# Optimization experiments

Measured on AMD Instinct MI355X. Metric: run time of the kernel, lower is better.

The kernel has to match this reference:

```python
import jax, jax.numpy as jnp
import numpy as np

N_NODES = 50000
N_EDGES = 800000
IN_DIM = 5
HID = (32, 64, 128, 64, 32)
OUT_DIM = 2
EPS = 1e-5  # nn.BatchNorm1d default eps


def _bn(x, g, b):
    # BatchNorm1d in training mode: batch (biased) statistics over nodes
    m = jnp.mean(x, axis=0)
    v = jnp.var(x, axis=0)
    return (x - m) * jax.lax.rsqrt(v + EPS) * g + b


def setup_inputs() -> dict:
    key = jax.random.key(0)
    ks = jax.random.split(key, 40)
    it = iter(range(40))
    def nrm(shape, s=0.1):
        return jax.random.normal(ks[next(it)], shape, jnp.float32) * s
    inp = {}
    inp["x"] = jax.random.normal(ks[next(it)], (N_NODES, IN_DIM), jnp.float32)
    inp["edge_index"] = jax.random.randint(ks[next(it)], (2, N_EDGES), 0, N_NODES, jnp.int32)
    # input embedding: Linear(5,32) -> ReLU -> BatchNorm1d(32)
    inp["emb_W"] = nrm((IN_DIM, HID[0]))
    inp["emb_b"] = jnp.zeros((HID[0],), jnp.float32)
    inp["emb_g"] = jnp.ones((HID[0],), jnp.float32)
    inp["emb_beta"] = jnp.zeros((HID[0],), jnp.float32)
    # 4 GraphConv blocks
    for i in range(len(HID) - 1):
        din, dout = HID[i], HID[i + 1]
        inp[f"b{i}_Wrel"] = nrm((din, dout))   # lin_rel weight (has bias)
        inp[f"b{i}_brel"] = jnp.zeros((dout,), jnp.float32)
        inp[f"b{i}_Wroot"] = nrm((din, dout))  # lin_root weight (no bias)
        inp[f"b{i}_g"] = jnp.ones((dout,), jnp.float32)
        inp[f"b{i}_beta"] = jnp.zeros((dout,), jnp.float32)
    # output MLP: Linear(32,16) -> ReLU -> Linear(16,2)
    inp["out_W1"] = nrm((HID[-1], HID[-1] // 2))
    inp["out_b1"] = jnp.zeros((HID[-1] // 2,), jnp.float32)
    inp["out_W2"] = nrm((HID[-1] // 2, OUT_DIM))
    inp["out_b2"] = jnp.zeros((OUT_DIM,), jnp.float32)
    return inp


def reference(x, edge_index,
              emb_W, emb_b, emb_g, emb_beta,
              b0_Wrel, b0_brel, b0_Wroot, b0_g, b0_beta,
              b1_Wrel, b1_brel, b1_Wroot, b1_g, b1_beta,
              b2_Wrel, b2_brel, b2_Wroot, b2_g, b2_beta,
              b3_Wrel, b3_brel, b3_Wroot, b3_g, b3_beta,
              out_W1, out_b1, out_W2, out_b2):
    src, dst = edge_index[0], edge_index[1]
    # input embedding: Linear -> ReLU -> BN
    h = jnp.maximum(x @ emb_W + emb_b, 0.0)
    h = _bn(h, emb_g, emb_beta)
    blocks = [
        (b0_Wrel, b0_brel, b0_Wroot, b0_g, b0_beta),
        (b1_Wrel, b1_brel, b1_Wroot, b1_g, b1_beta),
        (b2_Wrel, b2_brel, b2_Wroot, b2_g, b2_beta),
        (b3_Wrel, b3_brel, b3_Wroot, b3_g, b3_beta),
    ]
    for Wrel, brel, Wroot, g, beta in blocks:
        # GraphConv (aggr='add'): lin_rel(sum_{j in N(i)} x_j) + lin_root(x_i)
        agg = jax.ops.segment_sum(h[src], dst, num_segments=N_NODES)
        h = agg @ Wrel + brel + h @ Wroot
        # BN then ReLU (GNNBlock order)
        h = jnp.maximum(_bn(h, g, beta), 0.0)
    # output MLP
    h = jnp.maximum(h @ out_W1 + out_b1, 0.0)
    return h @ out_W2 + out_b2
```

## Files before the change

### kernel.cpp

```cpp
#include <hip/hip_runtime.h>

#define N_NODES 50000
#define N_EDGES 800000
#define BN_EPS 1e-5f

__device__ __forceinline__ void fma4(float4& a, float s, const float4& w) {
    a.x += s * w.x; a.y += s * w.y; a.z += s * w.z; a.w += s * w.w;
}
__device__ __forceinline__ void add4(float4& a, const float4& b) {
    a.x += b.x; a.y += b.y; a.z += b.z; a.w += b.w;
}

template <int NY>
__device__ __forceinline__ bool xcd_decode(int nx, int& x, int& y) {
    const int s = blockIdx.x & (8 * NY - 1);
    const int g = blockIdx.x / (8 * NY);
    x = g * 8 + (s & 7);
    y = s >> 3;
    return x < nx;
}
static inline int xcd_grid(int nx, int ny) { return ((nx + 7) / 8 * 8) * ny; }

__global__ void zero_i(int* __restrict__ p, int n) {
    int i = blockIdx.x * blockDim.x + threadIdx.x;
    int stride = gridDim.x * blockDim.x;
    for (; i < n; i += stride) p[i] = 0;
}

__global__ void hist_kernel(const int* __restrict__ dst, int* __restrict__ cnt) {
    int i = blockIdx.x * blockDim.x + threadIdx.x;
    int stride = gridDim.x * blockDim.x;
    for (; i < N_EDGES; i += stride) atomicAdd(&cnt[dst[i]], 1);
}
__global__ void scan1_kernel(const int* __restrict__ cnt, int* __restrict__ rp,
                             int* __restrict__ bsum) {
    __shared__ int s[256];
    int t = threadIdx.x;
    int idx = blockIdx.x * 256 + t;
    int v = (idx < N_NODES) ? cnt[idx] : 0;
    s[t] = v;
    __syncthreads();
    for (int off = 1; off < 256; off <<= 1) {
        int x = 0;
        if (t >= off) x = s[t - off];
        __syncthreads();
        s[t] += x;
        __syncthreads();
    }
    if (idx < N_NODES) rp[idx] = s[t] - v;
    if (t == 255) bsum[blockIdx.x] = s[255];
}
__global__ void scan2_kernel(int* __restrict__ bsum, int nb, float* __restrict__ stats) {
    __shared__ int s[256];
    int t = threadIdx.x;
    for (int i = t; i < 5 * 256; i += 256) stats[i] = 0.f;
    int v = (t < nb) ? bsum[t] : 0;
    s[t] = v;
    __syncthreads();
    for (int off = 1; off < 256; off <<= 1) {
        int x = 0;
        if (t >= off) x = s[t - off];
        __syncthreads();
        s[t] += x;
        __syncthreads();
    }
    if (t < nb) bsum[t] = s[t] - v;
}
__global__ void scan3_kernel(int* __restrict__ rp, const int* __restrict__ bsum,
                             int* __restrict__ cnt) {
    int idx = blockIdx.x * 256 + threadIdx.x;
    if (idx < N_NODES) {
        rp[idx] += bsum[blockIdx.x];
        cnt[idx] = 0;
    }
    if (idx == 0) rp[N_NODES] = N_EDGES;
}
__global__ void fill_kernel(const int* __restrict__ src, const int* __restrict__ dst,
                            const int* __restrict__ rp, int* __restrict__ cur,
                            int* __restrict__ ssrc) {
    int i = blockIdx.x * blockDim.x + threadIdx.x;
    int stride = gridDim.x * blockDim.x;
    for (; i < N_EDGES; i += stride) {
        int d = dst[i];
        int p = rp[d] + atomicAdd(&cur[d], 1);
        ssrc[p] = src[i];
    }
}

__global__ __launch_bounds__(256) void emb_fused(
    const float* __restrict__ x, const float* __restrict__ W,
    const float* __restrict__ b, float* __restrict__ out,
    float* __restrict__ stats) {
    __shared__ float lsum[32], lssq[32];
    if (threadIdx.x < 32) { lsum[threadIdx.x] = 0.f; lssq[threadIdx.x] = 0.f; }
    __syncthreads();
    const int o = threadIdx.x & 31;
    const int total = N_NODES * 32;
    float mys = 0.f, myq = 0.f;
    for (int base = blockIdx.x * 256; base < total; base += gridDim.x * 256) {
        int idx = base + threadIdx.x;
        float acc = 0.f;
        if (idx < total) {
            int n = idx >> 5;
            const float* xr = x + n * 5;
            acc = b[o];
#pragma unroll
            for (int k = 0; k < 5; ++k) acc += xr[k] * W[k * 32 + o];
            acc = fmaxf(acc, 0.f);
            out[idx] = acc;
        }
        mys += acc;
        myq += acc * acc;
    }
    mys += __shfl_xor(mys, 32);
    myq += __shfl_xor(myq, 32);
    if ((threadIdx.x & 63) < 32) { atomicAdd(&lsum[o], mys); atomicAdd(&lssq[o], myq); }
    __syncthreads();
    if (threadIdx.x < 32) {
        atomicAdd(&stats[threadIdx.x], lsum[threadIdx.x]);
        atomicAdd(&stats[32 + threadIdx.x], lssq[threadIdx.x]);
    }
}

template <int D>
__device__ __forceinline__ void bn_finalize_lds(
    const float* __restrict__ stats, const float* __restrict__ g,
    const float* __restrict__ beta, float* sc, float* sh) {
    const float invN = 1.f / (float)N_NODES;
    for (int f = threadIdx.x; f < D; f += 256) {
        float m = stats[f] * invN;
        float var = stats[D + f] * invN - m * m;
        float a = g[f] * rsqrtf(var + BN_EPS);
        sc[f] = a;
        sh[f] = beta[f] - m * a;
    }
    __syncthreads();
}

__global__ __launch_bounds__(256) void bn_apply(
    float4* __restrict__ h, const float* __restrict__ g,
    const float* __restrict__ beta, const float* __restrict__ stats,
    int logD, int relu) {
    const int D = 1 << logD;
    const int total4 = N_NODES << (logD - 2);
    const float invN = 1.f / (float)N_NODES;
    int idx = blockIdx.x * blockDim.x + threadIdx.x;
    int stride = gridDim.x * blockDim.x;
    for (; idx < total4; idx += stride) {
        int f = (idx & ((D >> 2) - 1)) << 2;
        float4 v = h[idx];
        float* vp = (float*)&v;
#pragma unroll
        for (int c = 0; c < 4; ++c) {
            float m = stats[f + c] * invN;
            float var = stats[D + f + c] * invN - m * m;
            float y = (vp[c] - m) * rsqrtf(var + BN_EPS) * g[f + c] + beta[f + c];
            if (relu) y = fmaxf(y, 0.f);
            vp[c] = y;
        }
        h[idx] = v;
    }
}

template <int LOGD>
__global__ __launch_bounds__(256) void gather_agg(
    const float* __restrict__ h, const int* __restrict__ rp,
    const int* __restrict__ ssrc, float4* __restrict__ agg) {
    constexpr int QSH = LOGD - 2;
    int tid = blockIdx.x * 256 + threadIdx.x;
    int node = tid >> QSH;
    if (node >= N_NODES) return;
    int q = tid & ((1 << QSH) - 1);
    int e0 = rp[node], e1 = rp[node + 1];
    float4 acc = make_float4(0.f, 0.f, 0.f, 0.f);
    int e = e0;
    for (; e + 4 <= e1; e += 4) {
        int s0 = ssrc[e], s1 = ssrc[e + 1], s2 = ssrc[e + 2], s3 = ssrc[e + 3];
        float4 v0 = ((const float4*)(h + ((size_t)s0 << LOGD)))[q];
        float4 v1 = ((const float4*)(h + ((size_t)s1 << LOGD)))[q];
        float4 v2 = ((const float4*)(h + ((size_t)s2 << LOGD)))[q];
        float4 v3 = ((const float4*)(h + ((size_t)s3 << LOGD)))[q];
        add4(v0, v1); add4(v2, v3); add4(acc, v0); add4(acc, v2);
    }
    for (; e < e1; ++e) {
        float4 v = ((const float4*)(h + ((size_t)ssrc[e] << LOGD)))[q];
        add4(acc, v);
    }
    agg[tid] = acc;
}

template <int DIN, int DOUT, int OBL>
__global__ __launch_bounds__(256) void gconv_bn0(
    const float* __restrict__ h, const float* __restrict__ agg,
    const float* __restrict__ Wrel, const float* __restrict__ brel,
    const float* __restrict__ Wroot, float* __restrict__ out,
    const float* __restrict__ stats_in, const float* __restrict__ g_in,
    const float* __restrict__ beta_in, const int* __restrict__ deg,
    float* __restrict__ stats_out, int nx) {
    constexpr int NY = 2;
    constexpr int LPN = OBL / 4;
    constexpr int SLOTS = 256 / LPN;
    constexpr int NPT = 4;
    constexpr int KS = 8;
    constexpr int TOT4 = DIN * OBL / 4;
    int bx, by;
    if (!xcd_decode<NY>(nx, bx, by)) return;
    __shared__ __align__(16) float wl[2 * DIN * OBL];
    __shared__ __align__(16) float sc[DIN];
    __shared__ __align__(16) float sh[DIN];
    __shared__ float lsum[OBL], lssq[OBL];
    const int ob0 = by * OBL;
    for (int e4 = threadIdx.x; e4 < TOT4; e4 += 256) {
        int k = e4 / (OBL / 4);
        int j = (e4 % (OBL / 4)) * 4;
        ((float4*)wl)[e4] = *(const float4*)(Wrel + (size_t)k * DOUT + ob0 + j);
        ((float4*)wl)[TOT4 + e4] = *(const float4*)(Wroot + (size_t)k * DOUT + ob0 + j);
    }
    if (threadIdx.x < OBL) { lsum[threadIdx.x] = 0.f; lssq[threadIdx.x] = 0.f; }
    bn_finalize_lds<DIN>(stats_in, g_in, beta_in, sc, sh);

    const int q = threadIdx.x & (LPN - 1);
    const int slot = threadIdx.x / LPN;
    const int o0 = ob0 + q * 4;
    const int nbase = bx * (SLOTS * NPT) + slot;

    float degf[NPT];
#pragma unroll
    for (int i = 0; i < NPT; ++i) {
        int n = nbase + i * SLOTS;
        degf[i] = (n < N_NODES) ? (float)deg[n] : 0.f;
    }

    float4 bias = *(const float4*)(brel + o0);
    float4 acc[NPT];
#pragma unroll
    for (int i = 0; i < NPT; ++i) acc[i] = bias;

#pragma unroll 1
    for (int s = 0; s < DIN / KS; ++s) {
        const int k0 = s * KS;
        float4 s2[2] = {((const float4*)sc)[k0 / 4], ((const float4*)sc)[k0 / 4 + 1]};
        float4 t2[2] = {((const float4*)sh)[k0 / 4], ((const float4*)sh)[k0 / 4 + 1]};
        const float* scp = (const float*)s2;
        const float* shp = (const float*)t2;
        float4 hv[NPT][2], av[NPT][2];
#pragma unroll
        for (int i = 0; i < NPT; ++i) {
            int n = nbase + i * SLOTS;
            int nn = (n < N_NODES) ? n : 0;
            const float4* hr = (const float4*)(h + (size_t)nn * DIN + k0);
            const float4* ar = (const float4*)(agg + (size_t)nn * DIN + k0);
            hv[i][0] = hr[0]; hv[i][1] = hr[1];
            av[i][0] = ar[0]; av[i][1] = ar[1];
        }
#pragma unroll
        for (int kk = 0; kk < KS; ++kk) {
            float4 wr = *(const float4*)&wl[(k0 + kk) * OBL + q * 4];
            float4 wo = *(const float4*)&wl[DIN * OBL + (k0 + kk) * OBL + q * 4];
#pragma unroll
            for (int i = 0; i < NPT; ++i) {
                float a  = fmaf(((const float*)av[i])[kk], scp[kk], degf[i] * shp[kk]);
                float hh = fmaf(((const float*)hv[i])[kk], scp[kk], shp[kk]);
                fma4(acc[i], a, wr);
                fma4(acc[i], hh, wo);
            }
        }
    }
#pragma unroll
    for (int i = 0; i < NPT; ++i) {
        int n = nbase + i * SLOTS;
        if (n < N_NODES)
            *(float4*)(out + (size_t)n * DOUT + o0) = acc[i];
        else
            acc[i] = make_float4(0.f, 0.f, 0.f, 0.f);
    }
    float4 s4 = make_float4(0.f, 0.f, 0.f, 0.f);
    float4 q4 = make_float4(0.f, 0.f, 0.f, 0.f);
#pragma unroll
    for (int i = 0; i < NPT; ++i) {
        s4.x += acc[i].x; s4.y += acc[i].y; s4.z += acc[i].z; s4.w += acc[i].w;
        q4.x += acc[i].x * acc[i].x; q4.y += acc[i].y * acc[i].y;
        q4.z += acc[i].z * acc[i].z; q4.w += acc[i].w * acc[i].w;
    }
#pragma unroll
    for (int d = LPN; d < 64; d <<= 1) {
        s4.x += __shfl_xor(s4.x, d); s4.y += __shfl_xor(s4.y, d);
        s4.z += __shfl_xor(s4.z, d); s4.w += __shfl_xor(s4.w, d);
        q4.x += __shfl_xor(q4.x, d); q4.y += __shfl_xor(q4.y, d);
        q4.z += __shfl_xor(q4.z, d); q4.w += __shfl_xor(q4.w, d);
    }
    if ((threadIdx.x & 63) < LPN) {
        int c = q * 4;
        atomicAdd(&lsum[c + 0], s4.x); atomicAdd(&lsum[c + 1], s4.y);
        atomicAdd(&lsum[c + 2], s4.z); atomicAdd(&lsum[c + 3], s4.w);
        atomicAdd(&lssq[c + 0], q4.x); atomicAdd(&lssq[c + 1], q4.y);
        atomicAdd(&lssq[c + 2], q4.z); atomicAdd(&lssq[c + 3], q4.w);
    }
    __syncthreads();
    if (threadIdx.x < OBL) {
        atomicAdd(&stats_out[ob0 + threadIdx.x], lsum[threadIdx.x]);
        atomicAdd(&stats_out[DOUT + ob0 + threadIdx.x], lssq[threadIdx.x]);
    }
}

template <int DIN, int DOUT, int OBL>
__global__ __launch_bounds__(256) void gconv_lds(
    const float* __restrict__ h, const float* __restrict__ agg,
    const float* __restrict__ Wrel, const float* __restrict__ brel,
    const float* __restrict__ Wroot, float* __restrict__ out,
    float* __restrict__ stats_out, int nx) {
    constexpr int NY = DOUT / OBL;
    constexpr int LPN = OBL / 4;
    constexpr int SLOTS = 256 / LPN;
    constexpr int NPT = 4;
    constexpr int KS = 8;
    constexpr int TOT4 = DIN * OBL / 4;
    int bx, by;
    if (!xcd_decode<NY>(nx, bx, by)) return;
    __shared__ __align__(16) float wl[2 * DIN * OBL];
    __shared__ float lsum[OBL], lssq[OBL];
    const int ob0 = by * OBL;
    for (int e4 = threadIdx.x; e4 < TOT4; e4 += 256) {
        int k = e4 / (OBL / 4);
        int j = (e4 % (OBL / 4)) * 4;
        ((float4*)wl)[e4] = *(const float4*)(Wrel + (size_t)k * DOUT + ob0 + j);
        ((float4*)wl)[TOT4 + e4] = *(const float4*)(Wroot + (size_t)k * DOUT + ob0 + j);
    }
    if (threadIdx.x < OBL) { lsum[threadIdx.x] = 0.f; lssq[threadIdx.x] = 0.f; }
    __syncthreads();

    const int q = threadIdx.x & (LPN - 1);
    const int slot = threadIdx.x / LPN;
    const int o0 = ob0 + q * 4;
    const int nbase = bx * (SLOTS * NPT) + slot;

    float4 bias = *(const float4*)(brel + o0);
    float4 acc[NPT];
#pragma unroll
    for (int i = 0; i < NPT; ++i) acc[i] = bias;

#pragma unroll 1
    for (int s = 0; s < DIN / KS; ++s) {
        const int k0 = s * KS;
        float4 hv[NPT][2], av[NPT][2];
#pragma unroll
        for (int i = 0; i < NPT; ++i) {
            int n = nbase + i * SLOTS;
            int nn = (n < N_NODES) ? n : 0;
            const float4* hr = (const float4*)(h + (size_t)nn * DIN + k0);
            const float4* ar = (const float4*)(agg + (size_t)nn * DIN + k0);
            hv[i][0] = hr[0]; hv[i][1] = hr[1];
            av[i][0] = ar[0]; av[i][1] = ar[1];
        }
#pragma unroll
        for (int kk = 0; kk < KS; ++kk) {
            float4 wr = *(const float4*)&wl[(k0 + kk) * OBL + q * 4];
            float4 wo = *(const float4*)&wl[DIN * OBL + (k0 + kk) * OBL + q * 4];
#pragma unroll
            for (int i = 0; i < NPT; ++i) {
                fma4(acc[i], ((const float*)av[i])[kk], wr);
                fma4(acc[i], ((const float*)hv[i])[kk], wo);
            }
        }
    }
#pragma unroll
    for (int i = 0; i < NPT; ++i) {
        int n = nbase + i * SLOTS;
        if (n < N_NODES)
            *(float4*)(out + (size_t)n * DOUT + o0) = acc[i];
        else
            acc[i] = make_float4(0.f, 0.f, 0.f, 0.f);
    }
    float4 s4 = make_float4(0.f, 0.f, 0.f, 0.f);
    float4 q4 = make_float4(0.f, 0.f, 0.f, 0.f);
#pragma unroll
    for (int i = 0; i < NPT; ++i) {
        s4.x += acc[i].x; s4.y += acc[i].y; s4.z += acc[i].z; s4.w += acc[i].w;
        q4.x += acc[i].x * acc[i].x; q4.y += acc[i].y * acc[i].y;
        q4.z += acc[i].z * acc[i].z; q4.w += acc[i].w * acc[i].w;
    }
#pragma unroll
    for (int d = LPN; d < 64; d <<= 1) {
        s4.x += __shfl_xor(s4.x, d); s4.y += __shfl_xor(s4.y, d);
        s4.z += __shfl_xor(s4.z, d); s4.w += __shfl_xor(s4.w, d);
        q4.x += __shfl_xor(q4.x, d); q4.y += __shfl_xor(q4.y, d);
        q4.z += __shfl_xor(q4.z, d); q4.w += __shfl_xor(q4.w, d);
    }
    if ((threadIdx.x & 63) < LPN) {
        int c = q * 4;
        atomicAdd(&lsum[c + 0], s4.x); atomicAdd(&lsum[c + 1], s4.y);
        atomicAdd(&lsum[c + 2], s4.z); atomicAdd(&lsum[c + 3], s4.w);
        atomicAdd(&lssq[c + 0], q4.x); atomicAdd(&lssq[c + 1], q4.y);
        atomicAdd(&lssq[c + 2], q4.z); atomicAdd(&lssq[c + 3], q4.w);
    }
    __syncthreads();
    if (threadIdx.x < OBL) {
        atomicAdd(&stats_out[ob0 + threadIdx.x], lsum[threadIdx.x]);
        atomicAdd(&stats_out[DOUT + ob0 + threadIdx.x], lssq[threadIdx.x]);
    }
}

template <int DIN, int DOUT, int OBL>
__global__ __launch_bounds__(256) void prem_bn(
    const float* __restrict__ h, const float* __restrict__ Wrel,
    const float* __restrict__ brel, const float* __restrict__ Wroot,
    float* __restrict__ P, float* __restrict__ Q,
    const float* __restrict__ stats_in, const float* __restrict__ g_in,
    const float* __restrict__ beta_in, int nx) {
    constexpr int NY = DOUT / OBL;
    constexpr int LPN = OBL / 4;
    constexpr int SLOTS = 256 / LPN;
    constexpr int NPT = 4;
    constexpr int KS = 8;
    constexpr int TOT4 = DIN * OBL / 4;
    int bx, by;
    if (!xcd_decode<NY>(nx, bx, by)) return;
    __shared__ __align__(16) float wl[2 * DIN * OBL];
    __shared__ __align__(16) float sc[DIN];
    __shared__ __align__(16) float sh[DIN];
    const int ob0 = by * OBL;
    for (int e4 = threadIdx.x; e4 < TOT4; e4 += 256) {
        int k = e4 / (OBL / 4);
        int j = (e4 % (OBL / 4)) * 4;
        ((float4*)wl)[e4] = *(const float4*)(Wrel + (size_t)k * DOUT + ob0 + j);
        ((float4*)wl)[TOT4 + e4] = *(const float4*)(Wroot + (size_t)k * DOUT + ob0 + j);
    }
    bn_finalize_lds<DIN>(stats_in, g_in, beta_in, sc, sh);

    const int q = threadIdx.x & (LPN - 1);
    const int slot = threadIdx.x / LPN;
    const int o0 = ob0 + q * 4;
    const int nbase = bx * (SLOTS * NPT) + slot;

    float4 bias = *(const float4*)(brel + o0);
    float4 accp[NPT], accq[NPT];
#pragma unroll
    for (int i = 0; i < NPT; ++i) {
        accp[i] = make_float4(0.f, 0.f, 0.f, 0.f);
        accq[i] = bias;
    }

#pragma unroll 1
    for (int s = 0; s < DIN / KS; ++s) {
        const int k0 = s * KS;
        float4 s2[2] = {((const float4*)sc)[k0 / 4], ((const float4*)sc)[k0 / 4 + 1]};
        float4 t2[2] = {((const float4*)sh)[k0 / 4], ((const float4*)sh)[k0 / 4 + 1]};
        const float* scp = (const float*)s2;
        const float* shp = (const float*)t2;
        float4 hv[NPT][2];
#pragma unroll
        for (int i = 0; i < NPT; ++i) {
            int n = nbase + i * SLOTS;
            int nn = (n < N_NODES) ? n : 0;
            const float4* hr = (const float4*)(h + (size_t)nn * DIN + k0);
            hv[i][0] = hr[0]; hv[i][1] = hr[1];
        }
#pragma unroll
        for (int kk = 0; kk < KS; ++kk) {
            float4 wr = *(const float4*)&wl[(k0 + kk) * OBL + q * 4];
            float4 wo = *(const float4*)&wl[DIN * OBL + (k0 + kk) * OBL + q * 4];
#pragma unroll
            for (int i = 0; i < NPT; ++i) {
                float hh = fmaxf(fmaf(((const float*)hv[i])[kk], scp[kk], shp[kk]), 0.f);
                fma4(accp[i], hh, wr);
                fma4(accq[i], hh, wo);
            }
        }
    }
#pragma unroll
    for (int i = 0; i < NPT; ++i) {
        int n = nbase + i * SLOTS;
        if (n < N_NODES) {
            *(float4*)(P + (size_t)n * DOUT + o0) = accp[i];
            *(float4*)(Q + (size_t)n * DOUT + o0) = accq[i];
        }
    }
}

template <int LOGD>
__global__ __launch_bounds__(256) void gather_add_fused(
    const float* __restrict__ P, const int* __restrict__ rp,
    const int* __restrict__ ssrc, float4* __restrict__ out,
    float* __restrict__ stats) {
    constexpr int D = 1 << LOGD;
    constexpr int Q4 = D / 4;
    __shared__ float lsum[D], lssq[D];
    if (threadIdx.x < D) { lsum[threadIdx.x] = 0.f; lssq[threadIdx.x] = 0.f; }
    __syncthreads();

    const int total = N_NODES * Q4;
    const int q = threadIdx.x & (Q4 - 1);
    float4 mys = make_float4(0.f, 0.f, 0.f, 0.f);
    float4 myq = make_float4(0.f, 0.f, 0.f, 0.f);

    for (int base = blockIdx.x * 256; base < total; base += gridDim.x * 256) {
        int tid = base + threadIdx.x;
        float4 acc = make_float4(0.f, 0.f, 0.f, 0.f);
        if (tid < total) {
            int node = tid >> (LOGD - 2);
            int e0 = rp[node], e1 = rp[node + 1];
            acc = out[tid];
            int e = e0;
            for (; e + 4 <= e1; e += 4) {
                int s0 = ssrc[e], s1 = ssrc[e + 1], s2 = ssrc[e + 2], s3 = ssrc[e + 3];
                float4 v0 = ((const float4*)(P + ((size_t)s0 << LOGD)))[q];
                float4 v1 = ((const float4*)(P + ((size_t)s1 << LOGD)))[q];
                float4 v2 = ((const float4*)(P + ((size_t)s2 << LOGD)))[q];
                float4 v3 = ((const float4*)(P + ((size_t)s3 << LOGD)))[q];
                add4(v0, v1); add4(v2, v3); add4(acc, v0); add4(acc, v2);
            }
            for (; e < e1; ++e) {
                float4 v = ((const float4*)(P + ((size_t)ssrc[e] << LOGD)))[q];
                add4(acc, v);
            }
            out[tid] = acc;
        }
        mys.x += acc.x; mys.y += acc.y; mys.z += acc.z; mys.w += acc.w;
        myq.x += acc.x * acc.x; myq.y += acc.y * acc.y;
        myq.z += acc.z * acc.z; myq.w += acc.w * acc.w;
    }
#pragma unroll
    for (int d = Q4; d < 64; d <<= 1) {
        mys.x += __shfl_xor(mys.x, d); mys.y += __shfl_xor(mys.y, d);
        mys.z += __shfl_xor(mys.z, d); mys.w += __shfl_xor(mys.w, d);
        myq.x += __shfl_xor(myq.x, d); myq.y += __shfl_xor(myq.y, d);
        myq.z += __shfl_xor(myq.z, d); myq.w += __shfl_xor(myq.w, d);
    }
    if ((threadIdx.x & 63) < Q4) {
        atomicAdd(&lsum[4 * q + 0], mys.x); atomicAdd(&lsum[4 * q + 1], mys.y);
        atomicAdd(&lsum[4 * q + 2], mys.z); atomicAdd(&lsum[4 * q + 3], mys.w);
        atomicAdd(&lssq[4 * q + 0], myq.x); atomicAdd(&lssq[4 * q + 1], myq.y);
        atomicAdd(&lssq[4 * q + 2], myq.z); atomicAdd(&lssq[4 * q + 3], myq.w);
    }
    __syncthreads();
    if (threadIdx.x < D) {
        atomicAdd(&stats[threadIdx.x], lsum[threadIdx.x]);
        atomicAdd(&stats[D + threadIdx.x], lssq[threadIdx.x]);
    }
}

__global__ __launch_bounds__(256) void outmlp_kernel(
    const float* __restrict__ h, const float* __restrict__ stats,
    const float* __restrict__ g, const float* __restrict__ beta,
    const float* __restrict__ W1, const float* __restrict__ b1,
    const float* __restrict__ W2, const float* __restrict__ b2,
    float* __restrict__ out) {
    int n = blockIdx.x * 256 + threadIdx.x;
    if (n >= N_NODES) return;
    const float invN = 1.f / (float)N_NODES;
    const float4* hr4 = (const float4*)(h + (size_t)n * 32);
    float hv[32];
#pragma unroll
    for (int k4 = 0; k4 < 8; ++k4) {
        float4 v = hr4[k4];
        float* vp = (float*)&v;
#pragma unroll
        for (int c = 0; c < 4; ++c) {
            int f = 4 * k4 + c;
            float m = stats[f] * invN;
            float var = stats[32 + f] * invN - m * m;
            hv[f] = fmaxf((vp[c] - m) * rsqrtf(var + BN_EPS) * g[f] + beta[f], 0.f);
        }
    }
    float hid[16];
#pragma unroll
    for (int j = 0; j < 16; ++j) hid[j] = b1[j];
#pragma unroll
    for (int k = 0; k < 32; ++k) {
        float hk = hv[k];
#pragma unroll
        for (int j = 0; j < 16; ++j) hid[j] += hk * W1[k * 16 + j];
    }
    float o0 = b2[0], o1 = b2[1];
#pragma unroll
    for (int j = 0; j < 16; ++j) {
        float t = fmaxf(hid[j], 0.f);
        o0 += t * W2[j * 2 + 0];
        o1 += t * W2[j * 2 + 1];
    }
    out[n * 2 + 0] = o0;
    out[n * 2 + 1] = o1;
}

extern "C" void kernel_launch(void* const* d_in, const int* in_sizes, int n_in,
                              void* d_out, int out_size, void* d_ws, size_t ws_size,
                              hipStream_t stream) {
    const float* x        = (const float*)d_in[0];
    const int*   ei       = (const int*)d_in[1];
    const int*   src      = ei;
    const int*   dst      = ei + N_EDGES;
    const float* emb_W    = (const float*)d_in[2];
    const float* emb_b    = (const float*)d_in[3];
    const float* emb_g    = (const float*)d_in[4];
    const float* emb_beta = (const float*)d_in[5];
    const float* out_W1   = (const float*)d_in[26];
    const float* out_b1   = (const float*)d_in[27];
    const float* out_W2   = (const float*)d_in[28];
    const float* out_b2   = (const float*)d_in[29];

    float* ws = (float*)d_ws;
    const size_t HMAX = (size_t)N_NODES * 128;
    float* hA    = ws;
    float* hB    = ws + HMAX;
    float* P     = ws + 2 * HMAX;
    float* stats = ws + 2 * HMAX + (size_t)N_NODES * 64;
    int*   rp    = (int*)(stats + 5 * 256);
    int*   cnt   = rp + N_NODES + 1;
    int*   bsum  = cnt + N_NODES;
    int*   ssrc  = bsum + 256;

    float* st0 = stats;
    float* st1 = stats + 256;
    float* st2 = stats + 512;
    float* st3 = stats + 768;
    float* st4 = stats + 1024;

    const int BS = 256;
    const int NB = (N_NODES + BS - 1) / BS;

    zero_i<<<64, BS, 0, stream>>>(cnt, N_NODES);
    hist_kernel<<<1024, BS, 0, stream>>>(dst, cnt);
    scan1_kernel<<<NB, 256, 0, stream>>>(cnt, rp, bsum);
    scan2_kernel<<<1, 256, 0, stream>>>(bsum, NB, stats);
    scan3_kernel<<<NB, 256, 0, stream>>>(rp, bsum, cnt);
    fill_kernel<<<1024, BS, 0, stream>>>(src, dst, rp, cnt, ssrc);

    emb_fused<<<512, BS, 0, stream>>>(x, emb_W, emb_b, hA, st0);

    gather_agg<5><<<(N_NODES * 8 + BS - 1) / BS, BS, 0, stream>>>(hA, rp, ssrc, (float4*)P);
    {
        const int nx = (N_NODES + 127) / 128;
        gconv_bn0<32, 64, 32><<<xcd_grid(nx, 2), BS, 0, stream>>>(
            hA, P, (const float*)d_in[6], (const float*)d_in[7], (const float*)d_in[8], hB,
            st0, emb_g, emb_beta, cnt, st1, nx);
    }
    bn_apply<<<2048, BS, 0, stream>>>((float4*)hB, (const float*)d_in[9], (const float*)d_in[10], st1, 6, 1);

    gather_agg<6><<<(N_NODES * 16 + BS - 1) / BS, BS, 0, stream>>>(hB, rp, ssrc, (float4*)P);
    {
        const int nx = (N_NODES + 127) / 128;
        gconv_lds<64, 128, 32><<<xcd_grid(nx, 4), BS, 0, stream>>>(
            hB, P, (const float*)d_in[11], (const float*)d_in[12], (const float*)d_in[13], hA, st2, nx);
    }

    {
        const int nx = (N_NODES + 255) / 256;
        prem_bn<128, 64, 16><<<xcd_grid(nx, 4), BS, 0, stream>>>(
            hA, (const float*)d_in[16], (const float*)d_in[17], (const float*)d_in[18], P, hB,
            st2, (const float*)d_in[14], (const float*)d_in[15], nx);
    }
    gather_add_fused<6><<<512, BS, 0, stream>>>(P, rp, ssrc, (float4*)hB, st3);

    {
        const int nx = (N_NODES + 255) / 256;
        prem_bn<64, 32, 16><<<xcd_grid(nx, 2), BS, 0, stream>>>(
            hB, (const float*)d_in[21], (const float*)d_in[22], (const float*)d_in[23], P, hA,
            st3, (const float*)d_in[19], (const float*)d_in[20], nx);
    }
    gather_add_fused<5><<<512, BS, 0, stream>>>(P, rp, ssrc, (float4*)hA, st4);

    outmlp_kernel<<<NB, BS, 0, stream>>>(
        hA, st4, (const float*)d_in[24], (const float*)d_in[25],
        out_W1, out_b1, out_W2, out_b2, (float*)d_out);
}
```

Baseline: 374.4 us.

## Store gathered node features in bf16 to halve edge-gather traffic

```diff
diff --git a/kernel.cpp b/kernel.cpp
--- a/kernel.cpp
+++ b/kernel.cpp
@@ -4,11 +4,30 @@
 #define N_EDGES 800000
 #define BN_EPS 1e-5f
 
+typedef unsigned int   u32;
+typedef unsigned short u16;
+
 __device__ __forceinline__ void fma4(float4& a, float s, const float4& w) {
     a.x += s * w.x; a.y += s * w.y; a.z += s * w.z; a.w += s * w.w;
 }
 __device__ __forceinline__ void add4(float4& a, const float4& b) {
     a.x += b.x; a.y += b.y; a.z += b.z; a.w += b.w;
+}
+__device__ __forceinline__ u16 f2bf(float f) {
+    union { u32 i; float f; } c; c.f = f;
+    return (u16)((c.i + 0x7FFFu + ((c.i >> 16) & 1u)) >> 16);
+}
+__device__ __forceinline__ float4 bf4(uint2 w) {
+    union { u32 i; float f; } a, b, c, d;
+    a.i = w.x << 16; b.i = w.x & 0xFFFF0000u;
+    c.i = w.y << 16; d.i = w.y & 0xFFFF0000u;
+    return make_float4(a.f, b.f, c.f, d.f);
+}
+__device__ __forceinline__ uint2 pack4(const float4& v) {
+    uint2 w;
+    w.x = (u32)f2bf(v.x) | ((u32)f2bf(v.y) << 16);
+    w.y = (u32)f2bf(v.z) | ((u32)f2bf(v.w) << 16);
+    return w;
 }
 
 template <int NY>
@@ -90,7 +109,7 @@
 __global__ __launch_bounds__(256) void emb_fused(
     const float* __restrict__ x, const float* __restrict__ W,
     const float* __restrict__ b, float* __restrict__ out,
-    float* __restrict__ stats) {
+    u16* __restrict__ out16, float* __restrict__ stats) {
     __shared__ float lsum[32], lssq[32];
     if (threadIdx.x < 32) { lsum[threadIdx.x] = 0.f; lssq[threadIdx.x] = 0.f; }
     __syncthreads();
@@ -108,6 +127,7 @@
             for (int k = 0; k < 5; ++k) acc += xr[k] * W[k * 32 + o];
             acc = fmaxf(acc, 0.f);
             out[idx] = acc;
+            out16[idx] = f2bf(acc);
         }
         mys += acc;
         myq += acc * acc;
@@ -137,10 +157,10 @@
     __syncthreads();
 }
 
-__global__ __launch_bounds__(256) void bn_apply(
-    float4* __restrict__ h, const float* __restrict__ g,
-    const float* __restrict__ beta, const float* __restrict__ stats,
-    int logD, int relu) {
+__global__ __launch_bounds__(256) void bn_apply16(
+    float4* __restrict__ h, u16* __restrict__ out16,
+    const float* __restrict__ g, const float* __restrict__ beta,
+    const float* __restrict__ stats, int logD) {
     const int D = 1 << logD;
     const int total4 = N_NODES << (logD - 2);
     const float invN = 1.f / (float)N_NODES;
@@ -154,17 +174,16 @@
         for (int c = 0; c < 4; ++c) {
             float m = stats[f + c] * invN;
             float var = stats[D + f + c] * invN - m * m;
-            float y = (vp[c] - m) * rsqrtf(var + BN_EPS) * g[f + c] + beta[f + c];
-            if (relu) y = fmaxf(y, 0.f);
-            vp[c] = y;
+            vp[c] = fmaxf((vp[c] - m) * rsqrtf(var + BN_EPS) * g[f + c] + beta[f + c], 0.f);
         }
         h[idx] = v;
+        ((uint2*)out16)[idx] = pack4(v);
     }
 }
 
 template <int LOGD>
-__global__ __launch_bounds__(256) void gather_agg(
-    const float* __restrict__ h, const int* __restrict__ rp,
+__global__ __launch_bounds__(256) void gather_agg_bf16(
+    const u16* __restrict__ h16, const int* __restrict__ rp,
     const int* __restrict__ ssrc, float4* __restrict__ agg) {
     constexpr int QSH = LOGD - 2;
     int tid = blockIdx.x * 256 + threadIdx.x;
@@ -176,14 +195,15 @@
     int e = e0;
     for (; e + 4 <= e1; e += 4) {
         int s0 = ssrc[e], s1 = ssrc[e + 1], s2 = ssrc[e + 2], s3 = ssrc[e + 3];
-        float4 v0 = ((const float4*)(h + ((size_t)s0 << LOGD)))[q];
-        float4 v1 = ((const float4*)(h + ((size_t)s1 << LOGD)))[q];
-        float4 v2 = ((const float4*)(h + ((size_t)s2 << LOGD)))[q];
-        float4 v3 = ((const float4*)(h + ((size_t)s3 << LOGD)))[q];
+        uint2 w0 = ((const uint2*)(h16 + ((size_t)s0 << LOGD)))[q];
+        uint2 w1 = ((const uint2*)(h16 + ((size_t)s1 << LOGD)))[q];
+        uint2 w2 = ((const uint2*)(h16 + ((size_t)s2 << LOGD)))[q];
+        uint2 w3 = ((const uint2*)(h16 + ((size_t)s3 << LOGD)))[q];
+        float4 v0 = bf4(w0), v1 = bf4(w1), v2 = bf4(w2), v3 = bf4(w3);
         add4(v0, v1); add4(v2, v3); add4(acc, v0); add4(acc, v2);
     }
     for (; e < e1; ++e) {
-        float4 v = ((const float4*)(h + ((size_t)ssrc[e] << LOGD)))[q];
+        float4 v = bf4(((const uint2*)(h16 + ((size_t)ssrc[e] << LOGD)))[q]);
         add4(acc, v);
     }
     agg[tid] = acc;
@@ -404,7 +424,7 @@
 __global__ __launch_bounds__(256) void prem_bn(
     const float* __restrict__ h, const float* __restrict__ Wrel,
     const float* __restrict__ brel, const float* __restrict__ Wroot,
-    float* __restrict__ P, float* __restrict__ Q,
+    u16* __restrict__ P16, float* __restrict__ Q,
     const float* __restrict__ stats_in, const float* __restrict__ g_in,
     const float* __restrict__ beta_in, int nx) {
     constexpr int NY = DOUT / OBL;
@@ -471,15 +491,15 @@
     for (int i = 0; i < NPT; ++i) {
         int n = nbase + i * SLOTS;
         if (n < N_NODES) {
-            *(float4*)(P + (size_t)n * DOUT + o0) = accp[i];
+            *(uint2*)(P16 + (size_t)n * DOUT + o0) = pack4(accp[i]);
             *(float4*)(Q + (size_t)n * DOUT + o0) = accq[i];
         }
     }
 }
 
 template <int LOGD>
-__global__ __launch_bounds__(256) void gather_add_fused(
-    const float* __restrict__ P, const int* __restrict__ rp,
+__global__ __launch_bounds__(256) void gather_add_bf16(
+    const u16* __restrict__ P16, const int* __restrict__ rp,
     const int* __restrict__ ssrc, float4* __restrict__ out,
     float* __restrict__ stats) {
     constexpr int D = 1 << LOGD;
@@ -503,14 +523,15 @@
             int e = e0;
             for (; e + 4 <= e1; e += 4) {
                 int s0 = ssrc[e], s1 = ssrc[e + 1], s2 = ssrc[e + 2], s3 = ssrc[e + 3];
-                float4 v0 = ((const float4*)(P + ((size_t)s0 << LOGD)))[q];
-                float4 v1 = ((const float4*)(P + ((size_t)s1 << LOGD)))[q];
-                float4 v2 = ((const float4*)(P + ((size_t)s2 << LOGD)))[q];
-                float4 v3 = ((const float4*)(P + ((size_t)s3 << LOGD)))[q];
+                uint2 w0 = ((const uint2*)(P16 + ((size_t)s0 << LOGD)))[q];
+                uint2 w1 = ((const uint2*)(P16 + ((size_t)s1 << LOGD)))[q];
+                uint2 w2 = ((const uint2*)(P16 + ((size_t)s2 << LOGD)))[q];
+                uint2 w3 = ((const uint2*)(P16 + ((size_t)s3 << LOGD)))[q];
+                float4 v0 = bf4(w0), v1 = bf4(w1), v2 = bf4(w2), v3 = bf4(w3);
                 add4(v0, v1); add4(v2, v3); add4(acc, v0); add4(acc, v2);
             }
             for (; e < e1; ++e) {
-                float4 v = ((const float4*)(P + ((size_t)ssrc[e] << LOGD)))[q];
+                float4 v = bf4(((const uint2*)(P16 + ((size_t)ssrc[e] << LOGD)))[q]);
                 add4(acc, v);
             }
             out[tid] = acc;
@@ -602,9 +623,11 @@
     const size_t HMAX = (size_t)N_NODES * 128;
     float* hA    = ws;
     float* hB    = ws + HMAX;
-    float* P     = ws + 2 * HMAX;
-    float* stats = ws + 2 * HMAX + (size_t)N_NODES * 64;
-    int*   rp    = (int*)(stats + 5 * 256);
+    float* AGG   = ws + 2 * HMAX;
+    u16*   P16   = (u16*)AGG;
+    float* stats = AGG + (size_t)N_NODES * 64;
+    u16*   h16   = (u16*)(stats + 5 * 256);
+    int*   rp    = (int*)(h16 + (size_t)N_NODES * 64);
     int*   cnt   = rp + N_NODES + 1;
     int*   bsum  = cnt + N_NODES;
     int*   ssrc  = bsum + 256;
@@ -625,39 +648,39 @@
     scan3_kernel<<<NB, 256, 0, stream>>>(rp, bsum, cnt);
     fill_kernel<<<1024, BS, 0, stream>>>(src, dst, rp, cnt, ssrc);
 
-    emb_fused<<<512, BS, 0, stream>>>(x, emb_W, emb_b, hA, st0);
-
-    gather_agg<5><<<(N_NODES * 8 + BS - 1) / BS, BS, 0, stream>>>(hA, rp, ssrc, (float4*)P);
+    emb_fused<<<512, BS, 0, stream>>>(x, emb_W, emb_b, hA, h16, st0);
+
+    gather_agg_bf16<5><<<(N_NODES * 8 + BS - 1) / BS, BS, 0, stream>>>(h16, rp, ssrc, (float4*)AGG);
     {
         const int nx = (N_NODES + 127) / 128;
         gconv_bn0<32, 64, 32><<<xcd_grid(nx, 2), BS, 0, stream>>>(
-            hA, P, (const float*)d_in[6], (const float*)d_in[7], (const float*)d_in[8], hB,
+            hA, AGG, (const float*)d_in[6], (const float*)d_in[7], (const float*)d_in[8], hB,
             st0, emb_g, emb_beta, cnt, st1, nx);
     }
-    bn_apply<<<2048, BS, 0, stream>>>((float4*)hB, (const float*)d_in[9], (const float*)d_in[10], st1, 6, 1);
-
-    gather_agg<6><<<(N_NODES * 16 + BS - 1) / BS, BS, 0, stream>>>(hB, rp, ssrc, (float4*)P);
+    bn_apply16<<<2048, BS, 0, stream>>>((float4*)hB, h16, (const float*)d_in[9], (const float*)d_in[10], st1, 6);
+
+    gather_agg_bf16<6><<<(N_NODES * 16 + BS - 1) / BS, BS, 0, stream>>>(h16, rp, ssrc, (float4*)AGG);
     {
         const int nx = (N_NODES + 127) / 128;
         gconv_lds<64, 128, 32><<<xcd_grid(nx, 4), BS, 0, stream>>>(
-            hB, P, (const float*)d_in[11], (const float*)d_in[12], (const float*)d_in[13], hA, st2, nx);
+            hB, AGG, (const float*)d_in[11], (const float*)d_in[12], (const float*)d_in[13], hA, st2, nx);
     }
 
     {
         const int nx = (N_NODES + 255) / 256;
         prem_bn<128, 64, 16><<<xcd_grid(nx, 4), BS, 0, stream>>>(
-            hA, (const float*)d_in[16], (const float*)d_in[17], (const float*)d_in[18], P, hB,
+            hA, (const float*)d_in[16], (const float*)d_in[17], (const float*)d_in[18], P16, hB,
             st2, (const float*)d_in[14], (const float*)d_in[15], nx);
     }
-    gather_add_fused<6><<<512, BS, 0, stream>>>(P, rp, ssrc, (float4*)hB, st3);
+    gather_add_bf16<6><<<512, BS, 0, stream>>>(P16, rp, ssrc, (float4*)hB, st3);
 
     {
         const int nx = (N_NODES + 255) / 256;
         prem_bn<64, 32, 16><<<xcd_grid(nx, 2), BS, 0, stream>>>(
-            hB, (const float*)d_in[21], (const float*)d_in[22], (const float*)d_in[23], P, hA,
+            hB, (const float*)d_in[21], (const float*)d_in[22], (const float*)d_in[23], P16, hA,
             st3, (const float*)d_in[19], (const float*)d_in[20], nx);
     }
-    gather_add_fused<5><<<512, BS, 0, stream>>>(P, rp, ssrc, (float4*)hA, st4);
+    gather_add_bf16<5><<<512, BS, 0, stream>>>(P16, rp, ssrc, (float4*)hA, st4);
 
     outmlp_kernel<<<NB, BS, 0, stream>>>(
         hA, st4, (const float*)d_in[24], (const float*)d_in[25],
```

Result: faster. 366.8 us (-2.0%).
